# Performance work log

Measured on AMD Instinct MI355X. Metric: run time of the kernel, lower is better.

The kernel has to match this reference:

```python
import jax, jax.numpy as jnp
import numpy as np

N_NODES = 100000
IN_DIM, HID_DIM, OUT_DIM = 512, 256, 64
N_EDGES = 3200000


def setup_inputs() -> dict:
    key = jax.random.key(0)
    k1, k2, k3, k4, k5 = jax.random.split(key, 5)
    x = jax.random.normal(k1, (N_NODES, IN_DIM), dtype=jnp.float32)
    W1 = jax.random.normal(k2, (IN_DIM, HID_DIM), dtype=jnp.float32) * (1.0 / np.sqrt(IN_DIM))
    W2 = jax.random.normal(k3, (HID_DIM, OUT_DIM), dtype=jnp.float32) * (1.0 / np.sqrt(HID_DIM))
    src = jax.random.randint(k4, (N_EDGES,), 0, N_NODES, dtype=jnp.int64)
    dst = jax.random.randint(k5, (N_EDGES,), 0, N_NODES, dtype=jnp.int64)
    edge_index = jnp.stack([src, dst], axis=0)
    return {"x": x, "W1": W1, "W2": W2, "edge_index": edge_index}


def _gcn_norm(edge_index, n):
    # add self loops, symmetric normalization deg^-1/2 A_hat deg^-1/2
    loop = jnp.arange(n, dtype=edge_index.dtype)
    src = jnp.concatenate([edge_index[0], loop])
    dst = jnp.concatenate([edge_index[1], loop])
    deg = jax.ops.segment_sum(jnp.ones_like(dst, dtype=jnp.float32), dst, num_segments=n)
    dinv = jnp.where(deg > 0, jax.lax.rsqrt(deg), 0.0)
    norm = dinv[src] * dinv[dst]  # [E + N]
    return src, dst, norm


def _gcn_layer(x, W, src, dst, norm, n):
    h = x @ W                       # dense projection [N, D_out]
    msg = h[src] * norm[:, None]    # gather + scale  [E+N, D_out]
    return jax.ops.segment_sum(msg, dst, num_segments=n)  # scatter-add [N, D_out]


def reference(x, W1, W2, edge_index):
    n = x.shape[0]
    src, dst, norm = _gcn_norm(edge_index, n)
    # dropout p=0.0 -> identity (inference reference)
    h = _gcn_layer(x, W1, src, dst, norm, n)
    h = jax.nn.relu(h)
    out = _gcn_layer(h, W2, src, dst, norm, n)
    return out
```

## Files before the change

### kernel.cpp

```cpp
#include <hip/hip_runtime.h>


typedef short s16x8 __attribute__((ext_vector_type(8)));
typedef float f32x4 __attribute__((ext_vector_type(4)));

static constexpr int IN_DIM = 512;
static constexpr int HID = 256;
static constexpr int OUTD = 64;

static constexpr int BKT_SHIFT = 8;
static constexpr int MAX_NB = 400;
static constexpr int CAP_BIN = 32;
static constexpr int EDGES_PER_BLOCK = 8192;
static constexpr int SEG_CAP = 16384;

static __device__ __forceinline__ float bf2f(unsigned short u) {
  unsigned int x = ((unsigned int)u) << 16;
  float f;
  __builtin_memcpy(&f, &x, 4);
  return f;
}
static __device__ __forceinline__ unsigned short f2bf(float f) {
  unsigned int x;
  __builtin_memcpy(&x, &f, 4);
  unsigned int r = x + 0x7fffu + ((x >> 16) & 1u);
  return (unsigned short)(r >> 16);
}

__global__ __launch_bounds__(256) void pack_init_kernel(
    const float* __restrict__ W1, const float* __restrict__ W2,
    short* __restrict__ Wt1, short* __restrict__ Wt2,
    unsigned* __restrict__ bucket_cursor) {
  int idx = blockIdx.x * blockDim.x + threadIdx.x;
  if (idx < IN_DIM * HID) {
    int n = idx / IN_DIM, k = idx - n * IN_DIM;
    Wt1[idx] = (short)f2bf(W1[(size_t)k * HID + n]);
  }
  if (idx < HID * OUTD) {
    int n = idx / HID, k = idx - n * HID;
    Wt2[idx] = (short)f2bf(W2[(size_t)k * OUTD + n]);
  }
  if (idx < 512) bucket_cursor[idx] = (unsigned)idx * SEG_CAP;
}

__global__ __launch_bounds__(256) void scatter_kernel(
    const int* __restrict__ src, const int* __restrict__ dst, int E,
    unsigned* __restrict__ bucket_cursor, unsigned* __restrict__ entry_buf) {
  __shared__ unsigned cnt[MAX_NB];
  __shared__ unsigned poss[MAX_NB];
  __shared__ unsigned buf[MAX_NB * CAP_BIN];
  const int tid = threadIdx.x;
  const int e0 = blockIdx.x * EDGES_PER_BLOCK;
  const int e1 = min(E, e0 + EDGES_PER_BLOCK);
  for (int i = tid; i < MAX_NB; i += 256) cnt[i] = 0;
  __syncthreads();
  for (int e = e0 + tid; e < e1; e += 256) {
    int d = dst[e];
    unsigned entry = (((unsigned)src[e]) << 8) | ((unsigned)d & 255u);
    int bkt = d >> BKT_SHIFT;
    unsigned slot = atomicAdd(&cnt[bkt], 1u);
    if (slot < CAP_BIN) {
      buf[bkt * CAP_BIN + slot] = entry;
    } else {
      unsigned pos = atomicAdd(&bucket_cursor[bkt], 1u);
      entry_buf[pos] = entry;
    }
  }
  __syncthreads();
  for (int b = tid; b < MAX_NB; b += 256) {
    unsigned c = min(cnt[b], (unsigned)CAP_BIN);
    poss[b] = c ? atomicAdd(&bucket_cursor[b], c) : 0u;
  }
  __syncthreads();
  for (int b0 = 0; b0 < MAX_NB; b0 += 8) {
    int b = b0 + (tid >> 5);
    int i = tid & 31;
    unsigned c = min(cnt[b], (unsigned)CAP_BIN);
    if ((unsigned)i < c) entry_buf[poss[b] + i] = buf[b * CAP_BIN + i];
  }
}

__global__ __launch_bounds__(256) void build_kernel(
    const unsigned* __restrict__ entry_buf,
    const unsigned* __restrict__ bucket_cursor, int Nn,
    int* __restrict__ csr_src, unsigned* __restrict__ row_start,
    unsigned* __restrict__ row_cnt, float* __restrict__ dinv) {
  __shared__ unsigned hist[256];
  __shared__ unsigned scn[256];
  const int tid = threadIdx.x;
  const int b = blockIdx.x;
  const unsigned nb0 = (unsigned)b * SEG_CAP;
  const int n_e = (int)(bucket_cursor[b] - nb0);

  hist[tid] = 0;
  __syncthreads();
  for (int i = tid; i < n_e; i += 256)
    atomicAdd(&hist[entry_buf[nb0 + i] & 255u], 1u);
  __syncthreads();

  unsigned v = hist[tid];
  scn[tid] = v;
  __syncthreads();
  for (int off = 1; off < 256; off <<= 1) {
    unsigned t = (tid >= off) ? scn[tid - off] : 0u;
    __syncthreads();
    scn[tid] += t;
    __syncthreads();
  }
  unsigned excl = scn[tid] - v;
  __syncthreads();
  scn[tid] = excl;

  int node = (b << BKT_SHIFT) + tid;
  if (node < Nn) {
    dinv[node] = rsqrtf((float)v + 1.0f);
    row_start[node] = nb0 + excl;
    row_cnt[node] = v;
  }
  hist[tid] = 0;
  __syncthreads();

  for (int i = tid; i < n_e; i += 256) {
    unsigned en = entry_buf[nb0 + i];
    unsigned d = en & 255u;
    unsigned r = atomicAdd(&hist[d], 1u);
    csr_src[nb0 + scn[d] + r] = (int)(en >> 8);
  }
}

template <int BM, int BN, int WGM, int WGN, bool A_F32>
__launch_bounds__(256)
__global__ void gemm_kernel(const void* __restrict__ Av,
                            const short* __restrict__ Bt,
                            short* __restrict__ C, int M, int K) {
  constexpr int BK = 32;
  constexpr int N = BN;
  __shared__ short sA[BM * BK];
  __shared__ short sB[BN * BK];
  const int tid = threadIdx.x;
  const int wave = tid >> 6, lane = tid & 63;
  const int lm = lane & 15, lq = lane >> 4;
  const int row0 = blockIdx.x * BM;
  const int wm0 = (WGM > 1) ? wave * 64 : 0;
  const int wn0 = (WGN > 1) ? wave * 64 : 0;

  f32x4 acc[4][4];
#pragma unroll
  for (int i = 0; i < 4; i++)
#pragma unroll
    for (int j = 0; j < 4; j++) acc[i][j] = f32x4{0.f, 0.f, 0.f, 0.f};

  for (int k0 = 0; k0 < K; k0 += BK) {
    if constexpr (A_F32) {
      static_assert(BM == 64, "fp32 A staging assumes BM=64");
      const float* A = (const float*)Av;
      int m = tid >> 2, kc = tid & 3;
      int row = row0 + m;
      float4 f0 = make_float4(0, 0, 0, 0), f1 = f0;
      if (row < M) {
        const float4* pa = (const float4*)(A + (size_t)row * K + k0 + kc * 8);
        f0 = pa[0];
        f1 = pa[1];
      }
      s16x8 v;
      v[0] = (short)f2bf(f0.x); v[1] = (short)f2bf(f0.y);
      v[2] = (short)f2bf(f0.z); v[3] = (short)f2bf(f0.w);
      v[4] = (short)f2bf(f1.x); v[5] = (short)f2bf(f1.y);
      v[6] = (short)f2bf(f1.z); v[7] = (short)f2bf(f1.w);
      *(s16x8*)&sA[m * BK + kc * 8] = v;
    } else {
      const short* A = (const short*)Av;
#pragma unroll
      for (int i = 0; i < BM / 64; i++) {
        int idx = tid + i * 256;
        int m = idx >> 2, kc = idx & 3;
        int row = row0 + m;
        s16x8 v = {0, 0, 0, 0, 0, 0, 0, 0};
        if (row < M) v = *(const s16x8*)(A + (size_t)row * K + k0 + kc * 8);
        *(s16x8*)&sA[m * BK + kc * 8] = v;
      }
    }
#pragma unroll
    for (int i = 0; i < BN / 64; i++) {
      int idx = tid + i * 256;
      int n = idx >> 2, kc = idx & 3;
      *(s16x8*)&sB[n * BK + kc * 8] =
          *(const s16x8*)(Bt + (size_t)n * K + k0 + kc * 8);
    }
    __syncthreads();

    s16x8 af[4], bfr[4];
#pragma unroll
    for (int mi = 0; mi < 4; mi++)
      af[mi] = *(const s16x8*)&sA[(wm0 + mi * 16 + lm) * BK + lq * 8];
#pragma unroll
    for (int ni = 0; ni < 4; ni++)
      bfr[ni] = *(const s16x8*)&sB[(wn0 + ni * 16 + lm) * BK + lq * 8];
#pragma unroll
    for (int mi = 0; mi < 4; mi++)
#pragma unroll
      for (int ni = 0; ni < 4; ni++)
        acc[mi][ni] = __builtin_amdgcn_mfma_f32_16x16x32_bf16(
            af[mi], bfr[ni], acc[mi][ni], 0, 0, 0);
    __syncthreads();
  }

#pragma unroll
  for (int mi = 0; mi < 4; mi++)
#pragma unroll
    for (int ni = 0; ni < 4; ni++)
#pragma unroll
      for (int r = 0; r < 4; r++) {
        int row = row0 + wm0 + mi * 16 + lq * 4 + r;
        int col = wn0 + ni * 16 + lm;
        if (row < M) C[(size_t)row * N + col] = (short)f2bf(acc[mi][ni][r]);
      }
}

__global__ __launch_bounds__(256) void agg1_kernel(
    const short* __restrict__ h1, const float* __restrict__ dinv,
    const unsigned* __restrict__ row_start, const unsigned* __restrict__ row_cnt,
    const int* __restrict__ csr_src, short* __restrict__ out, int n) {
  int node = blockIdx.x * 4 + (threadIdx.x >> 6);
  if (node >= n) return;
  const int lane = threadIdx.x & 63;
  const int half = lane >> 5;
  const int d0 = (lane & 31) * 8;
  const float di = dinv[node];
  float a[8];
#pragma unroll
  for (int j = 0; j < 8; j++) a[j] = 0.f;
  if (half == 0) {
    s16x8 v = *(const s16x8*)(h1 + (size_t)node * HID + d0);
    float ws = di * di;
#pragma unroll
    for (int j = 0; j < 8; j++) a[j] += bf2f((unsigned short)v[j]) * ws;
  }
  unsigned e = row_start[node] + half;
  const unsigned e1 = row_start[node] + row_cnt[node];
  for (; e + 6 < e1; e += 8) {
    int s0 = csr_src[e], s1 = csr_src[e + 2];
    int s2 = csr_src[e + 4], s3 = csr_src[e + 6];
    float w0 = dinv[s0] * di, w1 = dinv[s1] * di;
    float w2 = dinv[s2] * di, w3 = dinv[s3] * di;
    s16x8 v0 = *(const s16x8*)(h1 + (size_t)s0 * HID + d0);
    s16x8 v1 = *(const s16x8*)(h1 + (size_t)s1 * HID + d0);
    s16x8 v2 = *(const s16x8*)(h1 + (size_t)s2 * HID + d0);
    s16x8 v3 = *(const s16x8*)(h1 + (size_t)s3 * HID + d0);
#pragma unroll
    for (int j = 0; j < 8; j++)
      a[j] += bf2f((unsigned short)v0[j]) * w0 + bf2f((unsigned short)v1[j]) * w1 +
              bf2f((unsigned short)v2[j]) * w2 + bf2f((unsigned short)v3[j]) * w3;
  }
  for (; e < e1; e += 2) {
    int s0 = csr_src[e];
    float w0 = dinv[s0] * di;
    s16x8 v0 = *(const s16x8*)(h1 + (size_t)s0 * HID + d0);
#pragma unroll
    for (int j = 0; j < 8; j++) a[j] += bf2f((unsigned short)v0[j]) * w0;
  }
#pragma unroll
  for (int j = 0; j < 8; j++) a[j] += __shfl_xor(a[j], 32);
  if (half == 0) {
    s16x8 o;
#pragma unroll
    for (int j = 0; j < 8; j++) o[j] = (short)f2bf(fmaxf(a[j], 0.f));
    *(s16x8*)(out + (size_t)node * HID + d0) = o;
  }
}

__global__ __launch_bounds__(256) void agg2_kernel(
    const short* __restrict__ h2, const float* __restrict__ dinv,
    const unsigned* __restrict__ row_start, const unsigned* __restrict__ row_cnt,
    const int* __restrict__ csr_src, float* __restrict__ out, int n) {
  int node = blockIdx.x * 4 + (threadIdx.x >> 6);
  if (node >= n) return;
  const int lane = threadIdx.x & 63;
  const int q = lane >> 4;
  const int d0 = (lane & 15) * 4;
  const float di = dinv[node];
  float a[4] = {0.f, 0.f, 0.f, 0.f};
  if (q == 0) {
    ushort4 v = *(const ushort4*)(h2 + (size_t)node * OUTD + d0);
    float ws = di * di;
    a[0] = bf2f(v.x) * ws; a[1] = bf2f(v.y) * ws;
    a[2] = bf2f(v.z) * ws; a[3] = bf2f(v.w) * ws;
  }
  unsigned e = row_start[node] + q;
  const unsigned e1 = row_start[node] + row_cnt[node];
  for (; e + 4 < e1; e += 8) {
    int s0 = csr_src[e], s1 = csr_src[e + 4];
    float w0 = dinv[s0] * di, w1 = dinv[s1] * di;
    ushort4 v0 = *(const ushort4*)(h2 + (size_t)s0 * OUTD + d0);
    ushort4 v1 = *(const ushort4*)(h2 + (size_t)s1 * OUTD + d0);
    a[0] += bf2f(v0.x) * w0 + bf2f(v1.x) * w1;
    a[1] += bf2f(v0.y) * w0 + bf2f(v1.y) * w1;
    a[2] += bf2f(v0.z) * w0 + bf2f(v1.z) * w1;
    a[3] += bf2f(v0.w) * w0 + bf2f(v1.w) * w1;
  }
  for (; e < e1; e += 4) {
    int s0 = csr_src[e];
    float w0 = dinv[s0] * di;
    ushort4 v0 = *(const ushort4*)(h2 + (size_t)s0 * OUTD + d0);
    a[0] += bf2f(v0.x) * w0; a[1] += bf2f(v0.y) * w0;
    a[2] += bf2f(v0.z) * w0; a[3] += bf2f(v0.w) * w0;
  }
#pragma unroll
  for (int j = 0; j < 4; j++) {
    a[j] += __shfl_xor(a[j], 16);
    a[j] += __shfl_xor(a[j], 32);
  }
  if (q == 0) {
    float4 o = make_float4(a[0], a[1], a[2], a[3]);
    *(float4*)(out + (size_t)node * OUTD + d0) = o;
  }
}


extern "C" void kernel_launch(void* const* d_in, const int* in_sizes, int n_in,
                              void* d_out, int out_size, void* d_ws,
                              size_t ws_size, hipStream_t stream) {
  const float* x = (const float*)d_in[0];
  const float* W1 = (const float*)d_in[1];
  const float* W2 = (const float*)d_in[2];
  const int* ei = (const int*)d_in[3];
  const int E = in_sizes[3] / 2;
  const int Nn = in_sizes[0] / IN_DIM;
  const int* src = ei;
  const int* dst = ei + E;
  const int NB = (Nn + 255) >> BKT_SHIFT;

  char* p = (char*)d_ws;
  auto alloc = [&](size_t bytes) {
    char* r = p;
    p += (bytes + 255) & ~(size_t)255;
    return r;
  };
  unsigned* bucket_cursor = (unsigned*)alloc(512 * 4);
  unsigned* row_start = (unsigned*)alloc((size_t)Nn * 4);
  unsigned* row_cnt = (unsigned*)alloc((size_t)Nn * 4);
  float* dinv = (float*)alloc((size_t)Nn * 4);
  int* csr_src = (int*)alloc((size_t)MAX_NB * SEG_CAP * 4);
  unsigned* entry_buf = (unsigned*)alloc((size_t)MAX_NB * SEG_CAP * 4);
  short* Wt1 = (short*)alloc((size_t)IN_DIM * HID * 2);
  short* Wt2 = (short*)alloc((size_t)HID * OUTD * 2);
  short* h1 = (short*)alloc((size_t)Nn * HID * 2);
  short* agg1 = (short*)alloc((size_t)Nn * HID * 2);
  short* h2 = (short*)entry_buf;

  pack_init_kernel<<<(IN_DIM * HID + 255) / 256, 256, 0, stream>>>(
      W1, W2, Wt1, Wt2, bucket_cursor);
  scatter_kernel<<<(E + EDGES_PER_BLOCK - 1) / EDGES_PER_BLOCK, 256, 0,
                   stream>>>(src, dst, E, bucket_cursor, entry_buf);
  build_kernel<<<NB, 256, 0, stream>>>(entry_buf, bucket_cursor, Nn, csr_src,
                                       row_start, row_cnt, dinv);
  gemm_kernel<64, 256, 1, 4, true>
      <<<(Nn + 63) / 64, 256, 0, stream>>>(x, Wt1, h1, Nn, IN_DIM);
  agg1_kernel<<<(Nn + 3) / 4, 256, 0, stream>>>(h1, dinv, row_start, row_cnt,
                                                csr_src, agg1, Nn);
  gemm_kernel<256, 64, 4, 1, false>
      <<<(Nn + 255) / 256, 256, 0, stream>>>(agg1, Wt2, h2, Nn, HID);
  agg2_kernel<<<(Nn + 3) / 4, 256, 0, stream>>>(h2, dinv, row_start, row_cnt,
                                                csr_src, (float*)d_out, Nn);
}
```

Measured before the change: 707.8 us.

## Fold source-side degree scaling into GEMM epilogue and drop per-edge dinv gathers

Applies the dinv[src] normalization factor to each row in the GEMM epilogue, so the aggregation kernels sum plain neighbor rows and multiply by dinv[dst] once at the end. This removes a random dinv gather and a multiply per edge in both aggregation passes. It also doubles the unroll of the gather loops and adds an occupancy hint to the launch bounds. The trade-off is changed bf16 rounding order, since values are scaled before being rounded to bf16, plus possible register pressure from the wider unroll.

```diff
diff --git a/kernel.cpp b/kernel.cpp
--- a/kernel.cpp
+++ b/kernel.cpp
@@ -132,7 +132,8 @@
 __launch_bounds__(256)
 __global__ void gemm_kernel(const void* __restrict__ Av,
                             const short* __restrict__ Bt,
-                            short* __restrict__ C, int M, int K) {
+                            short* __restrict__ C, int M, int K,
+                            const float* __restrict__ dinv) {
   constexpr int BK = 32;
   constexpr int N = BN;
   __shared__ short sA[BM * BK];
@@ -208,16 +209,20 @@
 #pragma unroll
   for (int mi = 0; mi < 4; mi++)
 #pragma unroll
-    for (int ni = 0; ni < 4; ni++)
-#pragma unroll
-      for (int r = 0; r < 4; r++) {
-        int row = row0 + wm0 + mi * 16 + lq * 4 + r;
-        int col = wn0 + ni * 16 + lm;
-        if (row < M) C[(size_t)row * N + col] = (short)f2bf(acc[mi][ni][r]);
+    for (int r = 0; r < 4; r++) {
+      int row = row0 + wm0 + mi * 16 + lq * 4 + r;
+      if (row < M) {
+        float di = dinv[row];
+#pragma unroll
+        for (int ni = 0; ni < 4; ni++) {
+          int col = wn0 + ni * 16 + lm;
+          C[(size_t)row * N + col] = (short)f2bf(acc[mi][ni][r] * di);
+        }
       }
-}
-
-__global__ __launch_bounds__(256) void agg1_kernel(
+    }
+}
+
+__global__ __launch_bounds__(256, 8) void agg1_kernel(
     const short* __restrict__ h1, const float* __restrict__ dinv,
     const unsigned* __restrict__ row_start, const unsigned* __restrict__ row_cnt,
     const int* __restrict__ csr_src, short* __restrict__ out, int n) {
@@ -226,50 +231,66 @@
   const int lane = threadIdx.x & 63;
   const int half = lane >> 5;
   const int d0 = (lane & 31) * 8;
-  const float di = dinv[node];
   float a[8];
 #pragma unroll
   for (int j = 0; j < 8; j++) a[j] = 0.f;
   if (half == 0) {
     s16x8 v = *(const s16x8*)(h1 + (size_t)node * HID + d0);
-    float ws = di * di;
-#pragma unroll
-    for (int j = 0; j < 8; j++) a[j] += bf2f((unsigned short)v[j]) * ws;
+#pragma unroll
+    for (int j = 0; j < 8; j++) a[j] += bf2f((unsigned short)v[j]);
   }
   unsigned e = row_start[node] + half;
   const unsigned e1 = row_start[node] + row_cnt[node];
-  for (; e + 6 < e1; e += 8) {
+  for (; e + 14 < e1; e += 16) {
     int s0 = csr_src[e], s1 = csr_src[e + 2];
     int s2 = csr_src[e + 4], s3 = csr_src[e + 6];
-    float w0 = dinv[s0] * di, w1 = dinv[s1] * di;
-    float w2 = dinv[s2] * di, w3 = dinv[s3] * di;
+    int s4 = csr_src[e + 8], s5 = csr_src[e + 10];
+    int s6 = csr_src[e + 12], s7 = csr_src[e + 14];
     s16x8 v0 = *(const s16x8*)(h1 + (size_t)s0 * HID + d0);
     s16x8 v1 = *(const s16x8*)(h1 + (size_t)s1 * HID + d0);
     s16x8 v2 = *(const s16x8*)(h1 + (size_t)s2 * HID + d0);
     s16x8 v3 = *(const s16x8*)(h1 + (size_t)s3 * HID + d0);
+    s16x8 v4 = *(const s16x8*)(h1 + (size_t)s4 * HID + d0);
+    s16x8 v5 = *(const s16x8*)(h1 + (size_t)s5 * HID + d0);
+    s16x8 v6 = *(const s16x8*)(h1 + (size_t)s6 * HID + d0);
+    s16x8 v7 = *(const s16x8*)(h1 + (size_t)s7 * HID + d0);
 #pragma unroll
     for (int j = 0; j < 8; j++)
-      a[j] += bf2f((unsigned short)v0[j]) * w0 + bf2f((unsigned short)v1[j]) * w1 +
-              bf2f((unsigned short)v2[j]) * w2 + bf2f((unsigned short)v3[j]) * w3;
+      a[j] += ((bf2f((unsigned short)v0[j]) + bf2f((unsigned short)v1[j])) +
+               (bf2f((unsigned short)v2[j]) + bf2f((unsigned short)v3[j]))) +
+              ((bf2f((unsigned short)v4[j]) + bf2f((unsigned short)v5[j])) +
+               (bf2f((unsigned short)v6[j]) + bf2f((unsigned short)v7[j])));
+  }
+  for (; e + 6 < e1; e += 8) {
+    int s0 = csr_src[e], s1 = csr_src[e + 2];
+    int s2 = csr_src[e + 4], s3 = csr_src[e + 6];
+    s16x8 v0 = *(const s16x8*)(h1 + (size_t)s0 * HID + d0);
+    s16x8 v1 = *(const s16x8*)(h1 + (size_t)s1 * HID + d0);
+    s16x8 v2 = *(const s16x8*)(h1 + (size_t)s2 * HID + d0);
+    s16x8 v3 = *(const s16x8*)(h1 + (size_t)s3 * HID + d0);
+#pragma unroll
+    for (int j = 0; j < 8; j++)
+      a[j] += (bf2f((unsigned short)v0[j]) + bf2f((unsigned short)v1[j])) +
+              (bf2f((unsigned short)v2[j]) + bf2f((unsigned short)v3[j]));
   }
   for (; e < e1; e += 2) {
     int s0 = csr_src[e];
-    float w0 = dinv[s0] * di;
     s16x8 v0 = *(const s16x8*)(h1 + (size_t)s0 * HID + d0);
 #pragma unroll
-    for (int j = 0; j < 8; j++) a[j] += bf2f((unsigned short)v0[j]) * w0;
+    for (int j = 0; j < 8; j++) a[j] += bf2f((unsigned short)v0[j]);
   }
 #pragma unroll
   for (int j = 0; j < 8; j++) a[j] += __shfl_xor(a[j], 32);
   if (half == 0) {
+    const float di = dinv[node];
     s16x8 o;
 #pragma unroll
-    for (int j = 0; j < 8; j++) o[j] = (short)f2bf(fmaxf(a[j], 0.f));
+    for (int j = 0; j < 8; j++) o[j] = (short)f2bf(fmaxf(a[j] * di, 0.f));
     *(s16x8*)(out + (size_t)node * HID + d0) = o;
   }
 }
 
-__global__ __launch_bounds__(256) void agg2_kernel(
+__global__ __launch_bounds__(256, 8) void agg2_kernel(
     const short* __restrict__ h2, const float* __restrict__ dinv,
     const unsigned* __restrict__ row_start, const unsigned* __restrict__ row_cnt,
     const int* __restrict__ csr_src, float* __restrict__ out, int n) {
@@ -278,32 +299,30 @@
   const int lane = threadIdx.x & 63;
   const int q = lane >> 4;
   const int d0 = (lane & 15) * 4;
-  const float di = dinv[node];
   float a[4] = {0.f, 0.f, 0.f, 0.f};
   if (q == 0) {
     ushort4 v = *(const ushort4*)(h2 + (size_t)node * OUTD + d0);
-    float ws = di * di;
-    a[0] = bf2f(v.x) * ws; a[1] = bf2f(v.y) * ws;
-    a[2] = bf2f(v.z) * ws; a[3] = bf2f(v.w) * ws;
+    a[0] = bf2f(v.x); a[1] = bf2f(v.y); a[2] = bf2f(v.z); a[3] = bf2f(v.w);
   }
   unsigned e = row_start[node] + q;
   const unsigned e1 = row_start[node] + row_cnt[node];
-  for (; e + 4 < e1; e += 8) {
+  for (; e + 12 < e1; e += 16) {
     int s0 = csr_src[e], s1 = csr_src[e + 4];
-    float w0 = dinv[s0] * di, w1 = dinv[s1] * di;
+    int s2 = csr_src[e + 8], s3 = csr_src[e + 12];
     ushort4 v0 = *(const ushort4*)(h2 + (size_t)s0 * OUTD + d0);
     ushort4 v1 = *(const ushort4*)(h2 + (size_t)s1 * OUTD + d0);
-    a[0] += bf2f(v0.x) * w0 + bf2f(v1.x) * w1;
-    a[1] += bf2f(v0.y) * w0 + bf2f(v1.y) * w1;
-    a[2] += bf2f(v0.z) * w0 + bf2f(v1.z) * w1;
-    a[3] += bf2f(v0.w) * w0 + bf2f(v1.w) * w1;
+    ushort4 v2 = *(const ushort4*)(h2 + (size_t)s2 * OUTD + d0);
+    ushort4 v3 = *(const ushort4*)(h2 + (size_t)s3 * OUTD + d0);
+    a[0] += (bf2f(v0.x) + bf2f(v1.x)) + (bf2f(v2.x) + bf2f(v3.x));
+    a[1] += (bf2f(v0.y) + bf2f(v1.y)) + (bf2f(v2.y) + bf2f(v3.y));
+    a[2] += (bf2f(v0.z) + bf2f(v1.z)) + (bf2f(v2.z) + bf2f(v3.z));
+    a[3] += (bf2f(v0.w) + bf2f(v1.w)) + (bf2f(v2.w) + bf2f(v3.w));
   }
   for (; e < e1; e += 4) {
     int s0 = csr_src[e];
-    float w0 = dinv[s0] * di;
     ushort4 v0 = *(const ushort4*)(h2 + (size_t)s0 * OUTD + d0);
-    a[0] += bf2f(v0.x) * w0; a[1] += bf2f(v0.y) * w0;
-    a[2] += bf2f(v0.z) * w0; a[3] += bf2f(v0.w) * w0;
+    a[0] += bf2f(v0.x); a[1] += bf2f(v0.y);
+    a[2] += bf2f(v0.z); a[3] += bf2f(v0.w);
   }
 #pragma unroll
   for (int j = 0; j < 4; j++) {
@@ -311,7 +330,8 @@
     a[j] += __shfl_xor(a[j], 32);
   }
   if (q == 0) {
-    float4 o = make_float4(a[0], a[1], a[2], a[3]);
+    const float di = dinv[node];
+    float4 o = make_float4(a[0] * di, a[1] * di, a[2] * di, a[3] * di);
     *(float4*)(out + (size_t)node * OUTD + d0) = o;
   }
 }
@@ -355,11 +375,11 @@
   build_kernel<<<NB, 256, 0, stream>>>(entry_buf, bucket_cursor, Nn, csr_src,
                                        row_start, row_cnt, dinv);
   gemm_kernel<64, 256, 1, 4, true>
-      <<<(Nn + 63) / 64, 256, 0, stream>>>(x, Wt1, h1, Nn, IN_DIM);
+      <<<(Nn + 63) / 64, 256, 0, stream>>>(x, Wt1, h1, Nn, IN_DIM, dinv);
   agg1_kernel<<<(Nn + 3) / 4, 256, 0, stream>>>(h1, dinv, row_start, row_cnt,
                                                 csr_src, agg1, Nn);
   gemm_kernel<256, 64, 4, 1, false>
-      <<<(Nn + 255) / 256, 256, 0, stream>>>(agg1, Wt2, h2, Nn, HID);
+      <<<(Nn + 255) / 256, 256, 0, stream>>>(agg1, Wt2, h2, Nn, HID, dinv);
   agg2_kernel<<<(Nn + 3) / 4, 256, 0, stream>>>(h2, dinv, row_start, row_cnt,
                                                 csr_src, (float*)d_out, Nn);
 }
```

Result: slower. 730.7 us (+3.2%).
